# Kernel tuning notes

Hardware: AMD Instinct MI355X
Metric: run time of the kernel (lower is better)

The kernel has to match this reference:

```python
import jax, jax.numpy as jnp
import numpy as np


def setup_inputs() -> dict:
    key = jax.random.key(0)
    ks = jax.random.split(key, 7)
    N, E, F_in, H = 50000, 800000, 256, 128
    x = jax.random.normal(ks[0], (N, F_in), dtype=jnp.float32)
    edge_index = jax.random.randint(ks[1], (2, E), 0, N, dtype=jnp.int64)
    edge_weight = jax.random.uniform(ks[2], (E,), dtype=jnp.float32)
    W = jax.random.normal(ks[3], (H, F_in), dtype=jnp.float32) * 0.05
    b = jax.random.normal(ks[4], (H,), dtype=jnp.float32) * 0.05
    W_lin = jax.random.normal(ks[5], (2, H), dtype=jnp.float32) * 0.05
    b_lin = jax.random.normal(ks[6], (2,), dtype=jnp.float32) * 0.05
    return {"x": x, "edge_index": edge_index, "edge_weight": edge_weight,
            "W": W, "b": b, "W_lin": W_lin, "b_lin": b_lin}


def reference(x, edge_index, edge_weight, W, b, W_lin, b_lin):
    # GCNConv (PyG semantics): add self-loops (weight 1), symmetric gcn_norm,
    # linear transform, scatter-add aggregation at target, + bias.
    N = x.shape[0]
    loop = jnp.arange(N, dtype=edge_index.dtype)
    src = jnp.concatenate([edge_index[0], loop])  # [E+N]
    dst = jnp.concatenate([edge_index[1], loop])  # [E+N]
    w = jnp.concatenate([edge_weight, jnp.ones((N,), x.dtype)])  # [E+N]
    deg = jax.ops.segment_sum(w, dst, num_segments=N)  # [N]
    dinv = jnp.where(deg > 0, jax.lax.rsqrt(deg), 0.0)
    norm = dinv[src] * w * dinv[dst]  # [E+N]
    xw = x @ W.T  # [N, H] transform-then-gather (fewer FLOPs than gather-then-transform)
    msg = xw[src] * norm[:, None]  # [E+N, H]
    h = jax.ops.segment_sum(msg, dst, num_segments=N) + b  # [N, H]
    # dropout is identity in eval mode
    h = jax.nn.relu(h)
    out = h @ W_lin.T + b_lin  # [N, 2]
    return jax.nn.sigmoid(out)
```

## Files before the change

### kernel.cpp

```cpp
#include <hip/hip_runtime.h>

#define F_IN 256
#define H_DIM 128
#define BIN 64
#define CAP 2048
#define CH 4096

typedef short bf16x8 __attribute__((ext_vector_type(8)));
typedef float f32x4 __attribute__((ext_vector_type(4)));
typedef unsigned short ushort8 __attribute__((ext_vector_type(8)));

__device__ inline unsigned short f2bf(float f) {
    unsigned int u = __float_as_uint(f);
    u += 0x7fffu + ((u >> 16) & 1u);
    return (unsigned short)(u >> 16);
}
__device__ inline float bf_lo(unsigned int u) { return __uint_as_float(u << 16); }
__device__ inline float bf_hi(unsigned int u) { return __uint_as_float(u & 0xffff0000u); }

__global__ __launch_bounds__(256) void zero_cur_kernel(int* __restrict__ gcur, int nbins) {
    int i = blockIdx.x * blockDim.x + threadIdx.x;
    if (i < nbins) gcur[i] = 0;
}

__global__ __launch_bounds__(256) void bin_scatter_kernel(const int* __restrict__ ei,
                                                          const float* __restrict__ ew,
                                                          int* __restrict__ gcur,
                                                          int2* __restrict__ binned,
                                                          int E, int nbins) {
    __shared__ unsigned int bh[1024];
    __shared__ int bb[1024];
    __shared__ unsigned int bc[1024];
    int t = threadIdx.x, blk = blockIdx.x;
    for (int i = t; i < 1024; i += 256) { bh[i] = 0; bc[i] = 0; }
    __syncthreads();
    int e0 = blk * CH, e1 = min(e0 + CH, E);
    for (int i = e0 + t; i < e1; i += 256) atomicAdd(&bh[ei[(size_t)E + i] >> 6], 1u);
    __syncthreads();
    for (int b = t; b < nbins; b += 256) {
        int c = (int)bh[b];
        bb[b] = c ? atomicAdd(&gcur[b], c) : 0;
    }
    __syncthreads();
    for (int i = e0 + t; i < e1; i += 256) {
        int s = ei[i];
        int d = ei[(size_t)E + i];
        float wv = ew[i];
        int bin = d >> 6;
        int r = bb[bin] + (int)atomicAdd(&bc[bin], 1u);
        if (r < CAP) {
            int2 p;
            p.x = s | ((d & 63) << 16);
            p.y = __float_as_int(wv);
            binned[(size_t)bin * CAP + r] = p;
        }
    }
}

__global__ __launch_bounds__(256) void deg_bin_kernel(const int2* __restrict__ binned,
                                                      const int* __restrict__ gcur,
                                                      float* __restrict__ dinv, int N) {
    __shared__ unsigned int fx[BIN];
    int t = threadIdx.x, b = blockIdx.x;
    if (t < BIN) fx[t] = 0;
    __syncthreads();
    int ecnt = min(gcur[b], CAP);
    size_t ebase = (size_t)b * CAP;
    for (int i = t; i < ecnt; i += 256) {
        int2 p = binned[ebase + i];
        atomicAdd(&fx[(p.x >> 16) & 63],
                  (unsigned int)__float2uint_rn(__int_as_float(p.y) * 65536.0f));
    }
    __syncthreads();
    int node = b * BIN + t;
    if (t < BIN && node < N)
        dinv[node] = rsqrtf((float)fx[t] * (1.0f / 65536.0f) + 1.0f);
}

__global__ __launch_bounds__(256) void gemm_mfma_kernel(const float* __restrict__ x,
                                                        const float* __restrict__ W,
                                                        const float* __restrict__ dinv,
                                                        unsigned short* __restrict__ xs, int N) {
    __shared__ unsigned short As[64 * 64];
    __shared__ unsigned short Bs[128 * 64];
    __shared__ float sdinv[64];
    const int tid = threadIdx.x;
    const int wv = tid >> 6, lane = tid & 63;
    const int block_row = blockIdx.x * 64;
    if (tid < 64) {
        int gr = block_row + tid;
        sdinv[tid] = (gr < N) ? dinv[gr] : 0.0f;
    }
    f32x4 acc[8] = {};

    for (int ks = 0; ks < 4; ks++) {
#pragma unroll
        for (int it = 0; it < 2; it++) {
            int gg = it * 256 + tid;
            int row = gg >> 3, g = gg & 7;
            int gr = block_row + row;
            float4 v0 = {0, 0, 0, 0}, v1 = {0, 0, 0, 0};
            if (gr < N) {
                const float4* p = (const float4*)&x[(size_t)gr * F_IN + ks * 64 + g * 8];
                v0 = p[0]; v1 = p[1];
            }
            ushort8 o;
            o[0] = f2bf(v0.x); o[1] = f2bf(v0.y); o[2] = f2bf(v0.z); o[3] = f2bf(v0.w);
            o[4] = f2bf(v1.x); o[5] = f2bf(v1.y); o[6] = f2bf(v1.z); o[7] = f2bf(v1.w);
            int slot = g ^ (row & 7);
            *(ushort8*)&As[row * 64 + slot * 8] = o;
        }
#pragma unroll
        for (int it = 0; it < 4; it++) {
            int gg = it * 256 + tid;
            int col = gg >> 3, g = gg & 7;
            const float4* p = (const float4*)&W[(size_t)col * F_IN + ks * 64 + g * 8];
            float4 v0 = p[0], v1 = p[1];
            ushort8 o;
            o[0] = f2bf(v0.x); o[1] = f2bf(v0.y); o[2] = f2bf(v0.z); o[3] = f2bf(v0.w);
            o[4] = f2bf(v1.x); o[5] = f2bf(v1.y); o[6] = f2bf(v1.z); o[7] = f2bf(v1.w);
            int slot = g ^ (col & 7);
            *(ushort8*)&Bs[col * 64 + slot * 8] = o;
        }
        __syncthreads();
        {
            int lrow = wv * 16 + (lane & 15);
            int lgrp = lane >> 4;
#pragma unroll
            for (int c = 0; c < 2; c++) {
                int sA = (c * 4 + lgrp) ^ (lrow & 7);
                bf16x8 a = *(bf16x8*)&As[lrow * 64 + sA * 8];
#pragma unroll
                for (int j = 0; j < 8; j++) {
                    int col = j * 16 + (lane & 15);
                    int sB = (c * 4 + lgrp) ^ (col & 7);
                    bf16x8 bfr = *(bf16x8*)&Bs[col * 64 + sB * 8];
                    acc[j] = __builtin_amdgcn_mfma_f32_16x16x32_bf16(a, bfr, acc[j], 0, 0, 0);
                }
            }
        }
        __syncthreads();
    }

    const int lc = lane & 15;
#pragma unroll
    for (int j = 0; j < 8; j++) {
#pragma unroll
        for (int r = 0; r < 4; r++) {
            int lrow = wv * 16 + (lane >> 4) * 4 + r;
            int grow = block_row + lrow;
            if (grow < N) {
                float v = acc[j][r] * sdinv[lrow];
                xs[(size_t)grow * H_DIM + j * 16 + lc] = f2bf(v);
            }
        }
    }
}

__global__ __launch_bounds__(512) void bin_gather_kernel(const int2* __restrict__ binned,
                                                         const int* __restrict__ gcur,
                                                         const unsigned int* __restrict__ xs,
                                                         const float* __restrict__ dinv,
                                                         const float* __restrict__ b,
                                                         const float* __restrict__ Wl,
                                                         const float* __restrict__ bl,
                                                         float* __restrict__ out, int N) {
    __shared__ int2 se[CAP];
    __shared__ unsigned int cnt[BIN];
    __shared__ int nst[BIN + 1];
    int t = threadIdx.x, blk = blockIdx.x, lane = t & 63, wid = t >> 6;
    int node0 = blk * BIN;
    int ecnt = min(gcur[blk], CAP);
    size_t ebase = (size_t)blk * CAP;

    if (t < BIN) cnt[t] = 0;
    __syncthreads();
    for (int i = t; i < ecnt; i += 512)
        atomicAdd(&cnt[(binned[ebase + i].x >> 16) & 63], 1u);
    __syncthreads();
    if (t < BIN) {
        int v = (int)cnt[t];
        int s = v;
#pragma unroll
        for (int off = 1; off < 64; off <<= 1) {
            int tt = __shfl_up(s, off, 64);
            if (lane >= off) s += tt;
        }
        nst[t] = s - v;
        if (t == BIN - 1) nst[BIN] = s;
    }
    __syncthreads();
    if (t < BIN) cnt[t] = 0;
    __syncthreads();
    for (int i = t; i < ecnt; i += 512) {
        int2 p = binned[ebase + i];
        int dlo = (p.x >> 16) & 63;
        int r = (int)atomicAdd(&cnt[dlo], 1u);
        int2 o; o.x = p.x & 0xffff; o.y = p.y;
        se[nst[dlo] + r] = o;
    }
    __syncthreads();

    float2 bb2 = ((const float2*)b)[lane];
    float2 wl0 = ((const float2*)Wl)[lane];
    float2 wl1 = ((const float2*)(Wl + H_DIM))[lane];
    float bl0 = bl[0], bl1 = bl[1];
#pragma unroll 1
    for (int i = 0; i < 8; i++) {
        int node = wid * 8 + i;
        int gn = node0 + node;
        if (gn >= N) break;
        int js = nst[node], je = nst[node + 1];
        unsigned int su = xs[(size_t)gn * 64 + lane];
        float ax = bf_lo(su), ay = bf_hi(su);
        int j = js;
        for (; j + 8 <= je; j += 8) {
            int2 q0 = se[j],     q1 = se[j + 1], q2 = se[j + 2], q3 = se[j + 3];
            int2 q4 = se[j + 4], q5 = se[j + 5], q6 = se[j + 6], q7 = se[j + 7];
            unsigned int u0 = xs[(size_t)q0.x * 64 + lane];
            unsigned int u1 = xs[(size_t)q1.x * 64 + lane];
            unsigned int u2 = xs[(size_t)q2.x * 64 + lane];
            unsigned int u3 = xs[(size_t)q3.x * 64 + lane];
            unsigned int u4 = xs[(size_t)q4.x * 64 + lane];
            unsigned int u5 = xs[(size_t)q5.x * 64 + lane];
            unsigned int u6 = xs[(size_t)q6.x * 64 + lane];
            unsigned int u7 = xs[(size_t)q7.x * 64 + lane];
            float w0 = __int_as_float(q0.y), w1 = __int_as_float(q1.y);
            float w2 = __int_as_float(q2.y), w3 = __int_as_float(q3.y);
            float w4 = __int_as_float(q4.y), w5 = __int_as_float(q5.y);
            float w6 = __int_as_float(q6.y), w7 = __int_as_float(q7.y);
            ax += w0 * bf_lo(u0) + w1 * bf_lo(u1) + w2 * bf_lo(u2) + w3 * bf_lo(u3)
                + w4 * bf_lo(u4) + w5 * bf_lo(u5) + w6 * bf_lo(u6) + w7 * bf_lo(u7);
            ay += w0 * bf_hi(u0) + w1 * bf_hi(u1) + w2 * bf_hi(u2) + w3 * bf_hi(u3)
                + w4 * bf_hi(u4) + w5 * bf_hi(u5) + w6 * bf_hi(u6) + w7 * bf_hi(u7);
        }
        for (; j + 4 <= je; j += 4) {
            int2 q0 = se[j], q1 = se[j + 1], q2 = se[j + 2], q3 = se[j + 3];
            unsigned int u0 = xs[(size_t)q0.x * 64 + lane];
            unsigned int u1 = xs[(size_t)q1.x * 64 + lane];
            unsigned int u2 = xs[(size_t)q2.x * 64 + lane];
            unsigned int u3 = xs[(size_t)q3.x * 64 + lane];
            float w0 = __int_as_float(q0.y), w1 = __int_as_float(q1.y);
            float w2 = __int_as_float(q2.y), w3 = __int_as_float(q3.y);
            ax += w0 * bf_lo(u0) + w1 * bf_lo(u1) + w2 * bf_lo(u2) + w3 * bf_lo(u3);
            ay += w0 * bf_hi(u0) + w1 * bf_hi(u1) + w2 * bf_hi(u2) + w3 * bf_hi(u3);
        }
        for (; j < je; j++) {
            int2 q0 = se[j];
            unsigned int u0 = xs[(size_t)q0.x * 64 + lane];
            float w0 = __int_as_float(q0.y);
            ax += w0 * bf_lo(u0);
            ay += w0 * bf_hi(u0);
        }
        float di = dinv[gn];
        float r0 = fmaxf(ax * di + bb2.x, 0.0f);
        float r1 = fmaxf(ay * di + bb2.y, 0.0f);
        float z0 = r0 * wl0.x + r1 * wl0.y;
        float z1 = r0 * wl1.x + r1 * wl1.y;
#pragma unroll
        for (int off = 32; off; off >>= 1) {
            z0 += __shfl_xor(z0, off, 64);
            z1 += __shfl_xor(z1, off, 64);
        }
        if (lane == 0) {
            float2 o;
            o.x = 1.0f / (1.0f + expf(-(z0 + bl0)));
            o.y = 1.0f / (1.0f + expf(-(z1 + bl1)));
            ((float2*)out)[gn] = o;
        }
    }
}

extern "C" void kernel_launch(void* const* d_in, const int* in_sizes, int n_in,
                              void* d_out, int out_size, void* d_ws, size_t ws_size,
                              hipStream_t stream) {
    const float* x  = (const float*)d_in[0];
    const int* ei   = (const int*)d_in[1];
    const float* ew = (const float*)d_in[2];
    const float* W  = (const float*)d_in[3];
    const float* b  = (const float*)d_in[4];
    const float* Wl = (const float*)d_in[5];
    const float* bl = (const float*)d_in[6];
    float* out = (float*)d_out;

    const int N = in_sizes[0] / F_IN;
    const int E = in_sizes[2];
    const int nbins = (N + BIN - 1) / BIN;
    const int nblk  = (E + CH - 1) / CH;

    char* ws = (char*)d_ws;
    size_t off = 0;
    unsigned short* xs = (unsigned short*)(ws + off); off += (size_t)N * H_DIM * 2;
    int2* binned = (int2*)(ws + off); off += (size_t)nbins * CAP * 8;
    int* gcur    = (int*)(ws + off);  off += (size_t)nbins * 4;
    float* dinv  = (float*)(ws + off); off += (size_t)N * 4;

    zero_cur_kernel<<<(nbins + 255) / 256, 256, 0, stream>>>(gcur, nbins);
    bin_scatter_kernel<<<nblk, 256, 0, stream>>>(ei, ew, gcur, binned, E, nbins);
    deg_bin_kernel<<<nbins, 256, 0, stream>>>(binned, gcur, dinv, N);

    gemm_mfma_kernel<<<(N + 63) / 64, 256, 0, stream>>>(x, W, dinv, xs, N);

    bin_gather_kernel<<<nbins, 512, 0, stream>>>(binned, gcur,
                                                 (const unsigned int*)xs, dinv,
                                                 b, Wl, bl, out, N);
}
```

Baseline: 100.9 us.

## Fuse degree computation into GEMM and gather kernels, drop deg kernel

```diff
diff --git a/kernel.cpp b/kernel.cpp
--- a/kernel.cpp
+++ b/kernel.cpp
@@ -17,6 +17,9 @@
 }
 __device__ inline float bf_lo(unsigned int u) { return __uint_as_float(u << 16); }
 __device__ inline float bf_hi(unsigned int u) { return __uint_as_float(u & 0xffff0000u); }
+__device__ inline unsigned int wfx(int wbits) {
+    return (unsigned int)__float2uint_rn(__int_as_float(wbits) * 65536.0f);
+}
 
 __global__ __launch_bounds__(256) void zero_cur_kernel(int* __restrict__ gcur, int nbins) {
     int i = blockIdx.x * blockDim.x + threadIdx.x;
@@ -57,40 +60,32 @@
     }
 }
 
-__global__ __launch_bounds__(256) void deg_bin_kernel(const int2* __restrict__ binned,
-                                                      const int* __restrict__ gcur,
-                                                      float* __restrict__ dinv, int N) {
-    __shared__ unsigned int fx[BIN];
-    int t = threadIdx.x, b = blockIdx.x;
-    if (t < BIN) fx[t] = 0;
-    __syncthreads();
-    int ecnt = min(gcur[b], CAP);
-    size_t ebase = (size_t)b * CAP;
-    for (int i = t; i < ecnt; i += 256) {
-        int2 p = binned[ebase + i];
-        atomicAdd(&fx[(p.x >> 16) & 63],
-                  (unsigned int)__float2uint_rn(__int_as_float(p.y) * 65536.0f));
-    }
-    __syncthreads();
-    int node = b * BIN + t;
-    if (t < BIN && node < N)
-        dinv[node] = rsqrtf((float)fx[t] * (1.0f / 65536.0f) + 1.0f);
-}
-
 __global__ __launch_bounds__(256) void gemm_mfma_kernel(const float* __restrict__ x,
                                                         const float* __restrict__ W,
-                                                        const float* __restrict__ dinv,
+                                                        const int2* __restrict__ binned,
+                                                        const int* __restrict__ gcur,
                                                         unsigned short* __restrict__ xs, int N) {
     __shared__ unsigned short As[64 * 64];
     __shared__ unsigned short Bs[128 * 64];
+    __shared__ unsigned int fxg[64];
     __shared__ float sdinv[64];
     const int tid = threadIdx.x;
     const int wv = tid >> 6, lane = tid & 63;
     const int block_row = blockIdx.x * 64;
-    if (tid < 64) {
-        int gr = block_row + tid;
-        sdinv[tid] = (gr < N) ? dinv[gr] : 0.0f;
-    }
+
+    if (tid < 64) fxg[tid] = 0;
+    __syncthreads();
+    {
+        int ecnt = min(gcur[blockIdx.x], CAP);
+        size_t ebase = (size_t)blockIdx.x * CAP;
+        for (int i = tid; i < ecnt; i += 256) {
+            int2 p = binned[ebase + i];
+            atomicAdd(&fxg[(p.x >> 16) & 63], wfx(p.y));
+        }
+    }
+    __syncthreads();
+    if (tid < 64) sdinv[tid] = rsqrtf((float)fxg[tid] * (1.0f / 65536.0f) + 1.0f);
+
     f32x4 acc[8] = {};
 
     for (int ks = 0; ks < 4; ks++) {
@@ -160,23 +155,36 @@
 __global__ __launch_bounds__(512) void bin_gather_kernel(const int2* __restrict__ binned,
                                                          const int* __restrict__ gcur,
                                                          const unsigned int* __restrict__ xs,
-                                                         const float* __restrict__ dinv,
                                                          const float* __restrict__ b,
                                                          const float* __restrict__ Wl,
                                                          const float* __restrict__ bl,
                                                          float* __restrict__ out, int N) {
     __shared__ int2 se[CAP];
     __shared__ unsigned int cnt[BIN];
+    __shared__ unsigned int fx[BIN];
+    __shared__ float sdv[BIN];
     __shared__ int nst[BIN + 1];
     int t = threadIdx.x, blk = blockIdx.x, lane = t & 63, wid = t >> 6;
     int node0 = blk * BIN;
     int ecnt = min(gcur[blk], CAP);
     size_t ebase = (size_t)blk * CAP;
 
-    if (t < BIN) cnt[t] = 0;
-    __syncthreads();
-    for (int i = t; i < ecnt; i += 512)
-        atomicAdd(&cnt[(binned[ebase + i].x >> 16) & 63], 1u);
+    if (t < BIN) { cnt[t] = 0; fx[t] = 0; }
+    __syncthreads();
+
+    int2 eg0 = {0, 0}, eg1 = {0, 0}, eg2 = {0, 0}, eg3 = {0, 0};
+#pragma unroll
+    for (int k = 0; k < 4; k++) {
+        int i = t + k * 512;
+        if (i < ecnt) {
+            int2 e = binned[ebase + i];
+            int dlo = (e.x >> 16) & 63;
+            atomicAdd(&cnt[dlo], 1u);
+            atomicAdd(&fx[dlo], wfx(e.y));
+            if (k == 0) eg0 = e; else if (k == 1) eg1 = e;
+            else if (k == 2) eg2 = e; else eg3 = e;
+        }
+    }
     __syncthreads();
     if (t < BIN) {
         int v = (int)cnt[t];
@@ -188,16 +196,21 @@
         }
         nst[t] = s - v;
         if (t == BIN - 1) nst[BIN] = s;
+        sdv[t] = rsqrtf((float)fx[t] * (1.0f / 65536.0f) + 1.0f);
     }
     __syncthreads();
     if (t < BIN) cnt[t] = 0;
     __syncthreads();
-    for (int i = t; i < ecnt; i += 512) {
-        int2 p = binned[ebase + i];
-        int dlo = (p.x >> 16) & 63;
-        int r = (int)atomicAdd(&cnt[dlo], 1u);
-        int2 o; o.x = p.x & 0xffff; o.y = p.y;
-        se[nst[dlo] + r] = o;
+#pragma unroll
+    for (int k = 0; k < 4; k++) {
+        int i = t + k * 512;
+        if (i < ecnt) {
+            int2 e = (k == 0) ? eg0 : (k == 1) ? eg1 : (k == 2) ? eg2 : eg3;
+            int dlo = (e.x >> 16) & 63;
+            int r = (int)atomicAdd(&cnt[dlo], 1u);
+            int2 o; o.x = e.x & 0xffff; o.y = e.y;
+            se[nst[dlo] + r] = o;
+        }
     }
     __syncthreads();
 
@@ -214,6 +227,44 @@
         unsigned int su = xs[(size_t)gn * 64 + lane];
         float ax = bf_lo(su), ay = bf_hi(su);
         int j = js;
+        for (; j + 16 <= je; j += 16) {
+            int2 q0 = se[j],      q1 = se[j + 1],  q2 = se[j + 2],  q3 = se[j + 3];
+            int2 q4 = se[j + 4],  q5 = se[j + 5],  q6 = se[j + 6],  q7 = se[j + 7];
+            int2 q8 = se[j + 8],  q9 = se[j + 9],  qa = se[j + 10], qb = se[j + 11];
+            int2 qc = se[j + 12], qd = se[j + 13], qe = se[j + 14], qf = se[j + 15];
+            unsigned int u0 = xs[(size_t)q0.x * 64 + lane];
+            unsigned int u1 = xs[(size_t)q1.x * 64 + lane];
+            unsigned int u2 = xs[(size_t)q2.x * 64 + lane];
+            unsigned int u3 = xs[(size_t)q3.x * 64 + lane];
+            unsigned int u4 = xs[(size_t)q4.x * 64 + lane];
+            unsigned int u5 = xs[(size_t)q5.x * 64 + lane];
+            unsigned int u6 = xs[(size_t)q6.x * 64 + lane];
+            unsigned int u7 = xs[(size_t)q7.x * 64 + lane];
+            unsigned int u8 = xs[(size_t)q8.x * 64 + lane];
+            unsigned int u9 = xs[(size_t)q9.x * 64 + lane];
+            unsigned int ua = xs[(size_t)qa.x * 64 + lane];
+            unsigned int ub = xs[(size_t)qb.x * 64 + lane];
+            unsigned int uc = xs[(size_t)qc.x * 64 + lane];
+            unsigned int ud = xs[(size_t)qd.x * 64 + lane];
+            unsigned int ue = xs[(size_t)qe.x * 64 + lane];
+            unsigned int uf = xs[(size_t)qf.x * 64 + lane];
+            float w0 = __int_as_float(q0.y), w1 = __int_as_float(q1.y);
+            float w2 = __int_as_float(q2.y), w3 = __int_as_float(q3.y);
+            float w4 = __int_as_float(q4.y), w5 = __int_as_float(q5.y);
+            float w6 = __int_as_float(q6.y), w7 = __int_as_float(q7.y);
+            float w8 = __int_as_float(q8.y), w9 = __int_as_float(q9.y);
+            float wa = __int_as_float(qa.y), wb = __int_as_float(qb.y);
+            float wc = __int_as_float(qc.y), wd = __int_as_float(qd.y);
+            float we = __int_as_float(qe.y), wf = __int_as_float(qf.y);
+            ax += w0 * bf_lo(u0) + w1 * bf_lo(u1) + w2 * bf_lo(u2) + w3 * bf_lo(u3)
+                + w4 * bf_lo(u4) + w5 * bf_lo(u5) + w6 * bf_lo(u6) + w7 * bf_lo(u7)
+                + w8 * bf_lo(u8) + w9 * bf_lo(u9) + wa * bf_lo(ua) + wb * bf_lo(ub)
+                + wc * bf_lo(uc) + wd * bf_lo(ud) + we * bf_lo(ue) + wf * bf_lo(uf);
+            ay += w0 * bf_hi(u0) + w1 * bf_hi(u1) + w2 * bf_hi(u2) + w3 * bf_hi(u3)
+                + w4 * bf_hi(u4) + w5 * bf_hi(u5) + w6 * bf_hi(u6) + w7 * bf_hi(u7)
+                + w8 * bf_hi(u8) + w9 * bf_hi(u9) + wa * bf_hi(ua) + wb * bf_hi(ub)
+                + wc * bf_hi(uc) + wd * bf_hi(ud) + we * bf_hi(ue) + wf * bf_hi(uf);
+        }
         for (; j + 8 <= je; j += 8) {
             int2 q0 = se[j],     q1 = se[j + 1], q2 = se[j + 2], q3 = se[j + 3];
             int2 q4 = se[j + 4], q5 = se[j + 5], q6 = se[j + 6], q7 = se[j + 7];
@@ -252,7 +303,7 @@
             ax += w0 * bf_lo(u0);
             ay += w0 * bf_hi(u0);
         }
-        float di = dinv[gn];
+        float di = sdv[node];
         float r0 = fmaxf(ax * di + bb2.x, 0.0f);
         float r1 = fmaxf(ay * di + bb2.y, 0.0f);
         float z0 = r0 * wl0.x + r1 * wl0.y;
@@ -293,15 +344,13 @@
     unsigned short* xs = (unsigned short*)(ws + off); off += (size_t)N * H_DIM * 2;
     int2* binned = (int2*)(ws + off); off += (size_t)nbins * CAP * 8;
     int* gcur    = (int*)(ws + off);  off += (size_t)nbins * 4;
-    float* dinv  = (float*)(ws + off); off += (size_t)N * 4;
 
     zero_cur_kernel<<<(nbins + 255) / 256, 256, 0, stream>>>(gcur, nbins);
     bin_scatter_kernel<<<nblk, 256, 0, stream>>>(ei, ew, gcur, binned, E, nbins);
-    deg_bin_kernel<<<nbins, 256, 0, stream>>>(binned, gcur, dinv, N);
-
-    gemm_mfma_kernel<<<(N + 63) / 64, 256, 0, stream>>>(x, W, dinv, xs, N);
+
+    gemm_mfma_kernel<<<nbins, 256, 0, stream>>>(x, W, binned, gcur, xs, N);
 
     bin_gather_kernel<<<nbins, 512, 0, stream>>>(binned, gcur,
-                                                 (const unsigned int*)xs, dinv,
+                                                 (const unsigned int*)xs,
                                                  b, Wl, bl, out, N);
 }
```

After: 98.04 us. 2.8% less time.
